# Kernel optimization log

Hardware: AMD Instinct MI355X
Metric: run time of the kernel (lower is better)

Reference implementation:

```python
import jax, jax.numpy as jnp
import numpy as np

H = 768      # hidden_size
NH = 12      # num_attention_heads
DH = H // NH # attention_head_size
FF = 3072    # intermediate_size
E = 4        # n_expert
B, S = 8, 512
EPS = 1e-12


def _layernorm(x, g, b):
    mu = jnp.mean(x, axis=-1, keepdims=True)
    var = jnp.var(x, axis=-1, keepdims=True)
    return (x - mu) * jax.lax.rsqrt(var + EPS) * g + b


def _expert_linear(x, W, b, expert_idx):
    # W: [E, in, out], b: [E, out]; gather per-sample expert weights, then batched GEMM.
    # Mathematically identical to running every expert then slicing (single_select_fwd).
    Wg = W[expert_idx]            # [B, in, out]
    bg = b[expert_idx]            # [B, out]
    return jnp.einsum('bsi,bio->bso', x, Wg) + bg[:, None, :]


def setup_inputs() -> dict:
    key = jax.random.key(0)
    ks = jax.random.split(key, 16)
    sc = 0.02
    inp = {
        'hidden_states': jax.random.normal(ks[0], (B, S, H), jnp.float32),
        'expert_idx': jax.random.randint(ks[1], (B,), 0, E, jnp.int64) if jax.config.read('jax_enable_x64') else jax.random.randint(ks[1], (B,), 0, E).astype(jnp.int32),
        'attention_mask': jnp.zeros((B, 1, 1, S), jnp.float32),
        'Wq': sc * jax.random.normal(ks[2], (E, H, H), jnp.float32),
        'bq': jnp.zeros((E, H), jnp.float32),
        'Wk': sc * jax.random.normal(ks[3], (E, H, H), jnp.float32),
        'bk': jnp.zeros((E, H), jnp.float32),
        'Wv': sc * jax.random.normal(ks[4], (E, H, H), jnp.float32),
        'bv': jnp.zeros((E, H), jnp.float32),
        'Wo': sc * jax.random.normal(ks[5], (E, H, H), jnp.float32),
        'bo': jnp.zeros((E, H), jnp.float32),
        'ln1_g': jnp.ones((H,), jnp.float32),
        'ln1_b': jnp.zeros((H,), jnp.float32),
        'Wi': sc * jax.random.normal(ks[6], (E, H, FF), jnp.float32),
        'bi': jnp.zeros((E, FF), jnp.float32),
        'Wout': sc * jax.random.normal(ks[7], (E, FF, H), jnp.float32),
        'bout': jnp.zeros((E, H), jnp.float32),
        'ln2_g': jnp.ones((H,), jnp.float32),
        'ln2_b': jnp.zeros((H,), jnp.float32),
    }
    return inp


def reference(hidden_states, expert_idx, attention_mask, Wq, bq, Wk, bk, Wv, bv,
              Wo, bo, ln1_g, ln1_b, Wi, bi, Wout, bout, ln2_g, ln2_b):
    b, s, h = hidden_states.shape
    # --- MoE self-attention (per-sample expert QKV) ---
    q = _expert_linear(hidden_states, Wq, bq, expert_idx).reshape(b, s, NH, DH).transpose(0, 2, 1, 3)
    k = _expert_linear(hidden_states, Wk, bk, expert_idx).reshape(b, s, NH, DH).transpose(0, 2, 1, 3)
    v = _expert_linear(hidden_states, Wv, bv, expert_idx).reshape(b, s, NH, DH).transpose(0, 2, 1, 3)
    scores = jnp.einsum('bhqd,bhkd->bhqk', q, k) / np.sqrt(DH).astype(np.float32)
    scores = scores + attention_mask
    probs = jax.nn.softmax(scores, axis=-1)
    ctx = jnp.einsum('bhqk,bhkd->bhqd', probs, v).transpose(0, 2, 1, 3).reshape(b, s, h)
    # --- MoE self-output: dense + residual + LN ---
    attn_out = _expert_linear(ctx, Wo, bo, expert_idx)
    x = _layernorm(attn_out + hidden_states, ln1_g, ln1_b)
    # --- MoE FFN: intermediate (GELU) + output + residual + LN ---
    hmid = jax.nn.gelu(_expert_linear(x, Wi, bi, expert_idx), approximate=False)
    ffn = _expert_linear(hmid, Wout, bout, expert_idx)
    return _layernorm(ffn + x, ln2_g, ln2_b)
```

## Files before the change

kernel.cpp:

```cpp
#include <hip/hip_runtime.h>
#include <cstdint>
#include <cstddef>

constexpr int CB  = 8;
constexpr int CS  = 512;
constexpr int CH  = 768;
constexpr int CNH = 12;
constexpr int CDH = 64;
constexpr int CFF = 3072;
constexpr int CE  = 4;
constexpr int C3H = 3 * CH;

using f32x4  = __attribute__((ext_vector_type(4))) float;
using bf16x8 = __attribute__((ext_vector_type(8))) short;

__device__ __forceinline__ short f2bf(float x) {
  union { float f; uint32_t u; } v; v.f = x;
  return (short)((v.u + 0x7fffu + ((v.u >> 16) & 1u)) >> 16);
}

__device__ __forceinline__ void gload_lds16(const void* g, void* l) {
  __builtin_amdgcn_global_load_lds((const __attribute__((address_space(1))) void*)g,
                                   (__attribute__((address_space(3))) void*)l,
                                   16, 0, 0);
}

#define VMCNT(n)  asm volatile("s_waitcnt vmcnt(" #n ")" ::: "memory")
#define SCHEDB()  __builtin_amdgcn_sched_barrier(0)

__global__ void cvt_bf16_kernel(const float* __restrict__ in, short* __restrict__ out, int n4) {
  int i = blockIdx.x * blockDim.x + threadIdx.x;
  if (i < n4) {
    float4 v = ((const float4*)in)[i];
    short4 o;
    o.x = f2bf(v.x); o.y = f2bf(v.y); o.z = f2bf(v.z); o.w = f2bf(v.w);
    ((short4*)out)[i] = o;
  }
}

__device__ __forceinline__ bool expert_used(const int* __restrict__ eidx, int e) {
  bool u = false;
#pragma unroll
  for (int s = 0; s < CB; ++s) u |= (eidx[s] == e);
  return u;
}

__device__ __forceinline__ void tpose_body(const float* __restrict__ Wb,
                                           short* __restrict__ Wtb, int K, int N) {
  __shared__ __align__(16) short Ts[64 * 68];
  const int n0 = blockIdx.x * 64, k0 = blockIdx.y * 64;
  const int t  = threadIdx.x;
  const int tn = t & 15, tk = t >> 4;
#pragma unroll
  for (int p = 0; p < 4; ++p) {
    int k = k0 + p * 16 + tk;
    float4 v = *(const float4*)(Wb + (size_t)k * N + n0 + tn * 4);
#pragma unroll
    for (int j = 0; j < 4; ++j)
      Ts[(tn * 4 + j) * 68 + p * 16 + tk] = f2bf(((const float*)&v)[j]);
  }
  __syncthreads();
#pragma unroll
  for (int p = 0; p < 4; ++p) {
    int n = n0 + p * 16 + tk;
    uint2 o = *(const uint2*)(Ts + (p * 16 + tk) * 68 + tn * 4);
    *(uint2*)(Wtb + (size_t)n * K + k0 + tn * 4) = o;
  }
}

__global__ void tpose_cvt_kernel(const float* __restrict__ W, short* __restrict__ Wt,
                                 const int* __restrict__ eidx, int K, int N) {
  const int e = blockIdx.z;
  if (!expert_used(eidx, e)) return;
  tpose_body(W + (size_t)e * K * N, Wt + (size_t)e * K * N, K, N);
}

__global__ void tpose4_kernel(const float* __restrict__ Wq, const float* __restrict__ Wk,
                              const float* __restrict__ Wv, const float* __restrict__ Wo,
                              const int* __restrict__ eidx,
                              short* __restrict__ Wqkvt, short* __restrict__ Wot) {
  const int z = blockIdx.z, e = z >> 2, m = z & 3;
  if (!expert_used(eidx, e)) return;
  const float* W = (m == 0) ? Wq : (m == 1) ? Wk : (m == 2) ? Wv : Wo;
  const float* Wb = W + (size_t)e * CH * CH;
  short* dst = (m == 3) ? (Wot + (size_t)e * CH * CH)
                        : (Wqkvt + ((size_t)e * C3H + m * CH) * CH);
  tpose_body(Wb, dst, CH, CH);
}

__global__ void qkv_bias_kernel(const float* __restrict__ bq, const float* __restrict__ bk,
                                const float* __restrict__ bv, float* __restrict__ dst) {
  int i = blockIdx.x * 256 + threadIdx.x;
  if (i >= CE * C3H) return;
  int e = i / C3H, r = i % C3H;
  int m = r / CH, c = r % CH;
  const float* s = (m == 0) ? bq : (m == 1) ? bk : bv;
  dst[i] = s[e * CH + c];
}

template <int K, int NTN, int KSPLIT, int ACT, bool OB16>
__global__ __launch_bounds__(256, 2)
void gemm5_kernel(const short* __restrict__ A, const short* __restrict__ Wt,
                  const float* __restrict__ bias, const int* __restrict__ eidx,
                  char* __restrict__ out,
                  size_t wtExpStride, int biasStride, int outLd, size_t outKsStride) {
  constexpr int BM = 128, BN = 128, TPB = 256;
  constexpr int MI = 4;
  constexpr int NT = K / KSPLIT / 64;
  constexpr int JC = 4096 / BM;
  constexpr int MTS = CS / BM;
  __shared__ __align__(16) short As[2][BM * 64];
  __shared__ __align__(16) short Bs[2][BN * 64];
  const int t = threadIdx.x, w = t >> 6, l = t & 63, lr = l & 15, lg = l >> 4;

  int exv[CB];
#pragma unroll
  for (int s = 0; s < CB; ++s) exv[s] = eidx[s];
  uint32_t epack = 0;
#pragma unroll
  for (int s = 0; s < CB; ++s) epack |= (uint32_t)exv[s] << (2 * s);
  int c0 = 0, c1 = 0, c2 = 0;
#pragma unroll
  for (int s = 0; s < CB; ++s) {
    c0 += (exv[s] == 0); c1 += (exv[s] == 1); c2 += (exv[s] == 2);
  }
  int p0 = 0, p1 = c0, p2 = c0 + c1, p3 = c0 + c1 + c2;
  uint32_t sortedPack = 0;
#pragma unroll
  for (int s = 0; s < CB; ++s) {
    int e = exv[s];
    int p = (e == 0) ? p0 : (e == 1) ? p1 : (e == 2) ? p2 : p3;
    sortedPack |= (uint32_t)s << (4 * p);
    p0 += (e == 0); p1 += (e == 1); p2 += (e == 2); p3 += (e == 3);
  }
  const int chunk = (int)gridDim.x >> 3;
  const int W_ = ((int)blockIdx.x & 7) * chunk + ((int)blockIdx.x >> 3);
  const int ks = W_ / (JC * NTN);
  const int r1 = W_ - ks * (JC * NTN);
  const int j  = r1 / NTN, nt = r1 - j * NTN;
  const int sample = (int)((sortedPack >> (4 * (j / MTS))) & 7);
  const int jj = j % MTS;
  const int e  = (int)((epack >> (2 * sample)) & 3);
  const int mrow0 = sample * CS + jj * BM;
  const int kBase = ks * NT * 64;

  const int srow = t >> 3;
  const int gcol = (((t & 7) ^ ((t >> 3) & 7)) * 8);
  const short* aSrc = A + (size_t)(mrow0 + srow) * K + kBase + gcol;
  const short* bSrc = Wt + (size_t)e * wtExpStride + (size_t)(nt * BN + srow) * K + kBase + gcol;
  constexpr int RPI = TPB / 8;
  const size_t issStride = (size_t)RPI * K;

  const int wrow = (w >> 1) * 64, wn = (w & 1) * 64;
  int aoff[2][MI], boff[2][4];
#pragma unroll
  for (int kk = 0; kk < 2; ++kk) {
    const int slot = (kk * 4 + lg) ^ (lr & 7);
#pragma unroll
    for (int mi = 0; mi < MI; ++mi)
      aoff[kk][mi] = (wrow + mi * 16 + lr) * 64 + slot * 8;
#pragma unroll
    for (int ni = 0; ni < 4; ++ni)
      boff[kk][ni] = (wn + ni * 16 + lr) * 64 + slot * 8;
  }

  f32x4 acc[MI][4] = {};

  auto STAGE = [&](int buf, int kt) {
    const short* as = aSrc + (size_t)kt * 64;
#pragma unroll
    for (int i = 0; i < 4; ++i)
      gload_lds16(as + i * issStride, &As[buf][i * TPB * 8 + t * 8]);
    const short* bs = bSrc + (size_t)kt * 64;
#pragma unroll
    for (int i = 0; i < 4; ++i)
      gload_lds16(bs + i * issStride, &Bs[buf][i * TPB * 8 + t * 8]);
  };

  STAGE(0, 0);
  for (int kt = 0; kt < NT; ++kt) {
    const int buf = kt & 1;
    if (kt + 1 < NT) { STAGE(buf ^ 1, kt + 1); VMCNT(8); }
    else             { VMCNT(0); }
    __builtin_amdgcn_s_barrier();
    SCHEDB();
    bf16x8 af[2][MI], bfr[2][4];
#pragma unroll
    for (int kk = 0; kk < 2; ++kk) {
#pragma unroll
      for (int ni = 0; ni < 4; ++ni) bfr[kk][ni] = *(const bf16x8*)(&Bs[buf][boff[kk][ni]]);
#pragma unroll
      for (int mi = 0; mi < MI; ++mi) af[kk][mi] = *(const bf16x8*)(&As[buf][aoff[kk][mi]]);
    }
    __builtin_amdgcn_s_setprio(1);
#pragma unroll
    for (int kk = 0; kk < 2; ++kk)
#pragma unroll
      for (int mi = 0; mi < MI; ++mi)
#pragma unroll
        for (int ni = 0; ni < 4; ++ni)
          acc[mi][ni] = __builtin_amdgcn_mfma_f32_16x16x32_bf16(af[kk][mi], bfr[kk][ni],
                                                                acc[mi][ni], 0, 0, 0);
    __builtin_amdgcn_s_setprio(0);
    __builtin_amdgcn_s_barrier();
    SCHEDB();
  }

  float* outF = (float*)out + (size_t)ks * outKsStride;
#pragma unroll
  for (int ni = 0; ni < 4; ++ni) {
    const int col = nt * BN + wn + ni * 16 + lr;
    const float bv = bias ? bias[e * biasStride + col] : 0.0f;
#pragma unroll
    for (int mi = 0; mi < MI; ++mi) {
      const int row0 = mrow0 + wrow + mi * 16 + lg * 4;
#pragma unroll
      for (int r = 0; r < 4; ++r) {
        float v = acc[mi][ni][r] + bv;
        if (ACT == 1) v = 0.5f * v * (1.0f + erff(v * 0.70710678118654752f));
        if (OB16) ((short*)out)[(size_t)(row0 + r) * outLd + col] = f2bf(v);
        else      outF[(size_t)(row0 + r) * outLd + col] = v;
      }
    }
  }
}

__global__ void attn_kernel(const short* __restrict__ QKV, const float* __restrict__ mask,
                            short* __restrict__ ctx) {
  __shared__ __align__(16) short Vt[2][64 * 40];
  __shared__ __align__(16) short Pt[4][2][16 * 40];
  const int bh = blockIdx.x;
  const int b = bh / CNH, h = bh % CNH;
  const int qt = blockIdx.y;
  const int t = threadIdx.x, w = t >> 6, l = t & 63, lr = l & 15, lg = l >> 4;

  const size_t bS = (size_t)b * CS;
  const short* Qh = QKV + bS * C3H + h * CDH;
  const short* Kh = Qh + CH;
  const short* Vh = Qh + 2 * CH;
  const float* mrow = mask + bS;

  const int qrow = qt * 64 + w * 16 + lr;
  bf16x8 qa[2];
  qa[0] = *(const bf16x8*)(Qh + (size_t)qrow * C3H + lg * 8);
  qa[1] = *(const bf16x8*)(Qh + (size_t)qrow * C3H + 32 + lg * 8);

  f32x4 o[4] = {};
  float lp[4] = {0.f, 0.f, 0.f, 0.f};

  const int dh = t & 63, kg = t >> 6;
  {
    short v8[8];
#pragma unroll
    for (int j = 0; j < 8; ++j) v8[j] = Vh[(size_t)(kg * 8 + j) * C3H + dh];
    uint32_t p0 = (uint32_t)(uint16_t)v8[0] | ((uint32_t)(uint16_t)v8[1] << 16);
    uint32_t p1 = (uint32_t)(uint16_t)v8[2] | ((uint32_t)(uint16_t)v8[3] << 16);
    uint32_t p2 = (uint32_t)(uint16_t)v8[4] | ((uint32_t)(uint16_t)v8[5] << 16);
    uint32_t p3 = (uint32_t)(uint16_t)v8[6] | ((uint32_t)(uint16_t)v8[7] << 16);
    uint4 pk = {p0, p1, p2, p3};
    *(uint4*)(&Vt[0][dh * 40 + kg * 8]) = pk;
  }

  for (int tt = 0; tt < CS / 32; ++tt) {
    const int k0 = tt * 32;
    __syncthreads();

    f32x4 sacc[2] = {};
#pragma unroll
    for (int n = 0; n < 2; ++n) {
      bf16x8 kb0 = *(const bf16x8*)(Kh + (size_t)(k0 + n * 16 + lr) * C3H + lg * 8);
      bf16x8 kb1 = *(const bf16x8*)(Kh + (size_t)(k0 + n * 16 + lr) * C3H + 32 + lg * 8);
      sacc[n] = __builtin_amdgcn_mfma_f32_16x16x32_bf16(qa[0], kb0, sacc[n], 0, 0, 0);
      sacc[n] = __builtin_amdgcn_mfma_f32_16x16x32_bf16(qa[1], kb1, sacc[n], 0, 0, 0);
    }

    if (tt + 1 < CS / 32) {
      const int k1 = k0 + 32;
      short v8[8];
#pragma unroll
      for (int j = 0; j < 8; ++j) v8[j] = Vh[(size_t)(k1 + kg * 8 + j) * C3H + dh];
      uint32_t p0 = (uint32_t)(uint16_t)v8[0] | ((uint32_t)(uint16_t)v8[1] << 16);
      uint32_t p1 = (uint32_t)(uint16_t)v8[2] | ((uint32_t)(uint16_t)v8[3] << 16);
      uint32_t p2 = (uint32_t)(uint16_t)v8[4] | ((uint32_t)(uint16_t)v8[5] << 16);
      uint32_t p3 = (uint32_t)(uint16_t)v8[6] | ((uint32_t)(uint16_t)v8[7] << 16);
      uint4 pk = {p0, p1, p2, p3};
      *(uint4*)(&Vt[(tt + 1) & 1][dh * 40 + kg * 8]) = pk;
    }

    const int pb = tt & 1;
#pragma unroll
    for (int n = 0; n < 2; ++n) {
      float mv = mrow[k0 + n * 16 + lr];
#pragma unroll
      for (int r = 0; r < 4; ++r) {
        float s = sacc[n][r] * 0.125f + mv;
        float e = __expf(s);
        lp[r] += e;
        Pt[w][pb][(lg * 4 + r) * 40 + n * 16 + lr] = f2bf(e);
      }
    }

    bf16x8 pa = *(const bf16x8*)(&Pt[w][pb][lr * 40 + lg * 8]);
#pragma unroll
    for (int d = 0; d < 4; ++d) {
      bf16x8 vbf = *(const bf16x8*)(&Vt[tt & 1][(d * 16 + lr) * 40 + lg * 8]);
      o[d] = __builtin_amdgcn_mfma_f32_16x16x32_bf16(pa, vbf, o[d], 0, 0, 0);
    }
  }

#pragma unroll
  for (int r = 0; r < 4; ++r) {
    float s = lp[r];
    s += __shfl_xor(s, 1); s += __shfl_xor(s, 2);
    s += __shfl_xor(s, 4); s += __shfl_xor(s, 8);
    lp[r] = 1.0f / s;
  }
#pragma unroll
  for (int d = 0; d < 4; ++d)
#pragma unroll
    for (int r = 0; r < 4; ++r) {
      int row = qt * 64 + w * 16 + lg * 4 + r;
      ctx[(bS + row) * CH + h * CDH + d * 16 + lr] = f2bf(o[d][r] * lp[r]);
    }
}

__global__ void ln12_kernel(const float* __restrict__ p0, const float* __restrict__ p1,
                            const float* __restrict__ res,
                            const float* __restrict__ btab, const int* __restrict__ eidx,
                            const float* __restrict__ g, const float* __restrict__ bta,
                            float* __restrict__ out32, short* __restrict__ out16) {
  const int row = blockIdx.x;
  const int l = threadIdx.x;
  const int e = eidx[row >> 9];
  const float* xr0 = p0 + (size_t)row * CH;
  const float* xr1 = p1 + (size_t)row * CH;
  const float* rr  = res + (size_t)row * CH;
  const float* bo  = btab + (size_t)e * CH;
  float4 v[3];
  float sum = 0.f, ss = 0.f;
#pragma unroll
  for (int j = 0; j < 3; ++j) {
    float4 a = *(const float4*)(xr0 + j * 256 + l * 4);
    float4 c = *(const float4*)(xr1 + j * 256 + l * 4);
    float4 b = *(const float4*)(rr + j * 256 + l * 4);
    float4 bb = *(const float4*)(bo + j * 256 + l * 4);
    a.x += c.x + b.x + bb.x; a.y += c.y + b.y + bb.y;
    a.z += c.z + b.z + bb.z; a.w += c.w + b.w + bb.w;
    v[j] = a;
    sum += a.x + a.y + a.z + a.w;
    ss  += a.x * a.x + a.y * a.y + a.z * a.z + a.w * a.w;
  }
#pragma unroll
  for (int m = 1; m < 64; m <<= 1) { sum += __shfl_xor(sum, m); ss += __shfl_xor(ss, m); }
  const float mean = sum * (1.0f / CH);
  const float var  = ss * (1.0f / CH) - mean * mean;
  const float rstd = rsqrtf(var + 1e-12f);
#pragma unroll
  for (int j = 0; j < 3; ++j) {
    float4 gg = *(const float4*)(g   + j * 256 + l * 4);
    float4 bb = *(const float4*)(bta + j * 256 + l * 4);
    float4 a = v[j], y;
    y.x = (a.x - mean) * rstd * gg.x + bb.x;
    y.y = (a.y - mean) * rstd * gg.y + bb.y;
    y.z = (a.z - mean) * rstd * gg.z + bb.z;
    y.w = (a.w - mean) * rstd * gg.w + bb.w;
    *(float4*)(out32 + (size_t)row * CH + j * 256 + l * 4) = y;
    if (out16) {
      short4 o;
      o.x = f2bf(y.x); o.y = f2bf(y.y); o.z = f2bf(y.z); o.w = f2bf(y.w);
      *(short4*)(out16 + (size_t)row * CH + j * 256 + l * 4) = o;
    }
  }
}

extern "C" void kernel_launch(void* const* d_in, const int* in_sizes, int n_in,
                              void* d_out, int out_size, void* d_ws, size_t ws_size,
                              hipStream_t stream) {
  (void)in_sizes; (void)n_in; (void)out_size; (void)ws_size;
  const float* hidden = (const float*)d_in[0];
  const int*   eidx   = (const int*)d_in[1];
  const float* mask   = (const float*)d_in[2];
  const float* Wq   = (const float*)d_in[3];
  const float* bq   = (const float*)d_in[4];
  const float* Wk   = (const float*)d_in[5];
  const float* bk   = (const float*)d_in[6];
  const float* Wv   = (const float*)d_in[7];
  const float* bv   = (const float*)d_in[8];
  const float* Wo   = (const float*)d_in[9];
  const float* bo   = (const float*)d_in[10];
  const float* ln1g = (const float*)d_in[11];
  const float* ln1b = (const float*)d_in[12];
  const float* Wi   = (const float*)d_in[13];
  const float* bi   = (const float*)d_in[14];
  const float* Wout = (const float*)d_in[15];
  const float* bout = (const float*)d_in[16];
  const float* ln2g = (const float*)d_in[17];
  const float* ln2b = (const float*)d_in[18];

  char* ws = (char*)d_ws;
  size_t off = 0;
  auto alloc = [&](size_t bytes) {
    void* p = ws + off;
    off += (bytes + 255) & ~(size_t)255;
    return p;
  };
  const size_t M = (size_t)CB * CS;
  short* Xb    = (short*)alloc(M * CH * 2);
  char*  Rbig  = (char*)alloc(M * CFF * 2);
  char*  Rcx   = (char*)alloc(M * CH * 4);
  float* parts = (float*)alloc(2 * M * CH * 4);
  float* qkvbias = (float*)alloc(CE * C3H * 4);
  short* Wqkvt = (short*)alloc((size_t)CE * C3H * CH * 2);
  short* Wot   = (short*)alloc((size_t)CE * CH * CH * 2);
  short* Wit   = (short*)alloc((size_t)CE * CH * CFF * 2);
  short* Wo2t  = (short*)alloc((size_t)CE * CFF * CH * 2);
  short* QKVb = (short*)Rbig;
  short* hmid = (short*)Rbig;
  short* ctxb = (short*)Rcx;
  float* x1   = (float*)Rcx;
  short* x1b  = Xb;

  const int n4 = (int)(M * CH / 4);
  cvt_bf16_kernel<<<(n4 + 255) / 256, 256, 0, stream>>>(hidden, Xb, n4);
  tpose4_kernel<<<dim3(CH / 64, CH / 64, 4 * CE), 256, 0, stream>>>(Wq, Wk, Wv, Wo, eidx, Wqkvt, Wot);
  tpose_cvt_kernel<<<dim3(CFF / 64, CH / 64, CE), 256, 0, stream>>>(Wi, Wit, eidx, CH, CFF);
  tpose_cvt_kernel<<<dim3(CH / 64, CFF / 64, CE), 256, 0, stream>>>(Wout, Wo2t, eidx, CFF, CH);
  qkv_bias_kernel<<<(CE * C3H + 255) / 256, 256, 0, stream>>>(bq, bk, bv, qkvbias);

  gemm5_kernel<CH, 18, 1, 0, true><<<576, 256, 0, stream>>>(
      Xb, Wqkvt, qkvbias, eidx, (char*)QKVb, (size_t)C3H * CH, C3H, C3H, 0);
  attn_kernel<<<dim3(CB * CNH, CS / 64), 256, 0, stream>>>(QKVb, mask, ctxb);
  gemm5_kernel<CH, 6, 2, 0, false><<<384, 256, 0, stream>>>(
      ctxb, Wot, nullptr, eidx, (char*)parts, (size_t)CH * CH, CH, CH, M * CH);
  ln12_kernel<<<(int)M, 64, 0, stream>>>(parts, parts + M * CH, hidden, bo, eidx,
                                         ln1g, ln1b, x1, x1b);
  gemm5_kernel<CH, 24, 1, 1, true><<<768, 256, 0, stream>>>(
      x1b, Wit, bi, eidx, (char*)hmid, (size_t)CH * CFF, CFF, CFF, 0);
  gemm5_kernel<CFF, 6, 2, 0, false><<<384, 256, 0, stream>>>(
      hmid, Wo2t, nullptr, eidx, (char*)parts, (size_t)CFF * CH, CH, CH, M * CH);
  ln12_kernel<<<(int)M, 64, 0, stream>>>(parts, parts + M * CH, x1, bout, eidx,
                                         ln2g, ln2b, (float*)d_out, nullptr);
}
```

Before: 205.8 us.

## Add 128x256-tile triple-buffered GEMM kernel for QKV and FFN projections

Introduces gemm6, a 512-thread GEMM with 128x256 output tiles and a three-stage LDS pipeline that prefetches two k-tiles ahead. The QKV, FFN-intermediate and FFN-output GEMMs now use it, with half the grid size. The goal is more operand reuse per block and better hiding of global-load latency. In exchange it uses more LDS, runs one block per CU, and gives fewer blocks across the CUs, which may hurt wave balance, especially for the 192-block FFN-output GEMM. The expert-routing decode is factored into a shared helper.

New measurement: 221.8 us. +7.8%, slower.

```diff
diff --git a/kernel.cpp b/kernel.cpp
--- a/kernel.cpp
+++ b/kernel.cpp
@@ -98,6 +98,145 @@
   dst[i] = s[e * CH + c];
 }
 
+template <int BM, int NTN, int KSPLIT>
+__device__ __forceinline__ void moe_decode(const int* __restrict__ eidx,
+                                           int& e, int& mrow0, int& nt, int& ks) {
+  constexpr int JC = 4096 / BM;
+  constexpr int MTS = CS / BM;
+  int exv[CB];
+#pragma unroll
+  for (int s = 0; s < CB; ++s) exv[s] = eidx[s];
+  uint32_t epack = 0;
+#pragma unroll
+  for (int s = 0; s < CB; ++s) epack |= (uint32_t)exv[s] << (2 * s);
+  int c0 = 0, c1 = 0, c2 = 0;
+#pragma unroll
+  for (int s = 0; s < CB; ++s) {
+    c0 += (exv[s] == 0); c1 += (exv[s] == 1); c2 += (exv[s] == 2);
+  }
+  int p0 = 0, p1 = c0, p2 = c0 + c1, p3 = c0 + c1 + c2;
+  uint32_t sortedPack = 0;
+#pragma unroll
+  for (int s = 0; s < CB; ++s) {
+    int ee = exv[s];
+    int p = (ee == 0) ? p0 : (ee == 1) ? p1 : (ee == 2) ? p2 : p3;
+    sortedPack |= (uint32_t)s << (4 * p);
+    p0 += (ee == 0); p1 += (ee == 1); p2 += (ee == 2); p3 += (ee == 3);
+  }
+  const int chunk = (int)gridDim.x >> 3;
+  const int W_ = ((int)blockIdx.x & 7) * chunk + ((int)blockIdx.x >> 3);
+  ks = W_ / (JC * NTN);
+  const int r1 = W_ - ks * (JC * NTN);
+  const int j  = r1 / NTN; nt = r1 - j * NTN;
+  const int sample = (int)((sortedPack >> (4 * (j / MTS))) & 7);
+  const int jj = j % MTS;
+  e = (int)((epack >> (2 * sample)) & 3);
+  mrow0 = sample * CS + jj * BM;
+}
+
+template <int K, int NTN, int KSPLIT, int ACT, bool OB16>
+__global__ __launch_bounds__(512, 1)
+void gemm6_kernel(const short* __restrict__ A, const short* __restrict__ Wt,
+                  const float* __restrict__ bias, const int* __restrict__ eidx,
+                  char* __restrict__ out,
+                  size_t wtExpStride, int biasStride, int outLd, size_t outKsStride) {
+  constexpr int BM = 128, BN = 256;
+  constexpr int NT = K / KSPLIT / 64;
+  __shared__ __align__(16) short As[3][BM * 64];
+  __shared__ __align__(16) short Bs[3][BN * 64];
+  const int t = threadIdx.x, w = t >> 6, l = t & 63, lr = l & 15, lg = l >> 4;
+
+  int e, mrow0, nt, ks;
+  moe_decode<BM, NTN, KSPLIT>(eidx, e, mrow0, nt, ks);
+  const int kBase = ks * NT * 64;
+
+  const int srow = t >> 3;
+  const int gcol = (((t & 7) ^ ((t >> 3) & 7)) * 8);
+  const short* aSrc = A + (size_t)(mrow0 + srow) * K + kBase + gcol;
+  const short* bSrc = Wt + (size_t)e * wtExpStride + (size_t)(nt * BN + srow) * K + kBase + gcol;
+  const size_t iss64 = (size_t)64 * K;
+
+  const int wrow = (w >> 2) * 64, wn = (w & 3) * 64;
+  int aoff[2][4], boff[2][4];
+#pragma unroll
+  for (int kk = 0; kk < 2; ++kk) {
+    const int slot = (kk * 4 + lg) ^ (lr & 7);
+#pragma unroll
+    for (int mi = 0; mi < 4; ++mi)
+      aoff[kk][mi] = (wrow + mi * 16 + lr) * 64 + slot * 8;
+#pragma unroll
+    for (int ni = 0; ni < 4; ++ni)
+      boff[kk][ni] = (wn + ni * 16 + lr) * 64 + slot * 8;
+  }
+
+  f32x4 acc[4][4] = {};
+
+  auto STAGE = [&](int buf, int kt) {
+    const short* as = aSrc + (size_t)kt * 64;
+#pragma unroll
+    for (int i = 0; i < 2; ++i)
+      gload_lds16(as + i * iss64, &As[buf][i * 4096 + t * 8]);
+    const short* bs = bSrc + (size_t)kt * 64;
+#pragma unroll
+    for (int i = 0; i < 4; ++i)
+      gload_lds16(bs + i * iss64, &Bs[buf][i * 4096 + t * 8]);
+  };
+
+  STAGE(0, 0);
+  STAGE(1, 1);
+  VMCNT(6);
+  __builtin_amdgcn_s_barrier();
+  SCHEDB();
+
+  int cb = 0;
+  for (int kt = 0; kt < NT; ++kt) {
+    if (kt + 2 < NT) {
+      const int sb = (cb == 0) ? 2 : cb - 1;
+      STAGE(sb, kt + 2);
+    }
+#pragma unroll
+    for (int kk = 0; kk < 2; ++kk) {
+      bf16x8 af[4], bfr[4];
+#pragma unroll
+      for (int ni = 0; ni < 4; ++ni) bfr[ni] = *(const bf16x8*)(&Bs[cb][boff[kk][ni]]);
+#pragma unroll
+      for (int mi = 0; mi < 4; ++mi) af[mi] = *(const bf16x8*)(&As[cb][aoff[kk][mi]]);
+      __builtin_amdgcn_s_setprio(1);
+#pragma unroll
+      for (int mi = 0; mi < 4; ++mi)
+#pragma unroll
+        for (int ni = 0; ni < 4; ++ni)
+          acc[mi][ni] = __builtin_amdgcn_mfma_f32_16x16x32_bf16(af[mi], bfr[ni],
+                                                                acc[mi][ni], 0, 0, 0);
+      __builtin_amdgcn_s_setprio(0);
+    }
+    SCHEDB();
+    if (kt + 2 < NT) { VMCNT(6); }
+    else             { VMCNT(0); }
+    __builtin_amdgcn_s_barrier();
+    SCHEDB();
+    cb = (cb == 2) ? 0 : cb + 1;
+  }
+
+  float* outF = (float*)out + (size_t)ks * outKsStride;
+#pragma unroll
+  for (int ni = 0; ni < 4; ++ni) {
+    const int col = nt * BN + wn + ni * 16 + lr;
+    const float bv = bias ? bias[e * biasStride + col] : 0.0f;
+#pragma unroll
+    for (int mi = 0; mi < 4; ++mi) {
+      const int row0 = mrow0 + wrow + mi * 16 + lg * 4;
+#pragma unroll
+      for (int r = 0; r < 4; ++r) {
+        float v = acc[mi][ni][r] + bv;
+        if (ACT == 1) v = 0.5f * v * (1.0f + erff(v * 0.70710678118654752f));
+        if (OB16) ((short*)out)[(size_t)(row0 + r) * outLd + col] = f2bf(v);
+        else      outF[(size_t)(row0 + r) * outLd + col] = v;
+      }
+    }
+  }
+}
+
 template <int K, int NTN, int KSPLIT, int ACT, bool OB16>
 __global__ __launch_bounds__(256, 2)
 void gemm5_kernel(const short* __restrict__ A, const short* __restrict__ Wt,
@@ -107,41 +246,12 @@
   constexpr int BM = 128, BN = 128, TPB = 256;
   constexpr int MI = 4;
   constexpr int NT = K / KSPLIT / 64;
-  constexpr int JC = 4096 / BM;
-  constexpr int MTS = CS / BM;
   __shared__ __align__(16) short As[2][BM * 64];
   __shared__ __align__(16) short Bs[2][BN * 64];
   const int t = threadIdx.x, w = t >> 6, l = t & 63, lr = l & 15, lg = l >> 4;
 
-  int exv[CB];
-#pragma unroll
-  for (int s = 0; s < CB; ++s) exv[s] = eidx[s];
-  uint32_t epack = 0;
-#pragma unroll
-  for (int s = 0; s < CB; ++s) epack |= (uint32_t)exv[s] << (2 * s);
-  int c0 = 0, c1 = 0, c2 = 0;
-#pragma unroll
-  for (int s = 0; s < CB; ++s) {
-    c0 += (exv[s] == 0); c1 += (exv[s] == 1); c2 += (exv[s] == 2);
-  }
-  int p0 = 0, p1 = c0, p2 = c0 + c1, p3 = c0 + c1 + c2;
-  uint32_t sortedPack = 0;
-#pragma unroll
-  for (int s = 0; s < CB; ++s) {
-    int e = exv[s];
-    int p = (e == 0) ? p0 : (e == 1) ? p1 : (e == 2) ? p2 : p3;
-    sortedPack |= (uint32_t)s << (4 * p);
-    p0 += (e == 0); p1 += (e == 1); p2 += (e == 2); p3 += (e == 3);
-  }
-  const int chunk = (int)gridDim.x >> 3;
-  const int W_ = ((int)blockIdx.x & 7) * chunk + ((int)blockIdx.x >> 3);
-  const int ks = W_ / (JC * NTN);
-  const int r1 = W_ - ks * (JC * NTN);
-  const int j  = r1 / NTN, nt = r1 - j * NTN;
-  const int sample = (int)((sortedPack >> (4 * (j / MTS))) & 7);
-  const int jj = j % MTS;
-  const int e  = (int)((epack >> (2 * sample)) & 3);
-  const int mrow0 = sample * CS + jj * BM;
+  int e, mrow0, nt, ks;
+  moe_decode<BM, NTN, KSPLIT>(eidx, e, mrow0, nt, ks);
   const int kBase = ks * NT * 64;
 
   const int srow = t >> 3;
@@ -427,16 +537,16 @@
   tpose_cvt_kernel<<<dim3(CH / 64, CFF / 64, CE), 256, 0, stream>>>(Wout, Wo2t, eidx, CFF, CH);
   qkv_bias_kernel<<<(CE * C3H + 255) / 256, 256, 0, stream>>>(bq, bk, bv, qkvbias);
 
-  gemm5_kernel<CH, 18, 1, 0, true><<<576, 256, 0, stream>>>(
+  gemm6_kernel<CH, 9, 1, 0, true><<<288, 512, 0, stream>>>(
       Xb, Wqkvt, qkvbias, eidx, (char*)QKVb, (size_t)C3H * CH, C3H, C3H, 0);
   attn_kernel<<<dim3(CB * CNH, CS / 64), 256, 0, stream>>>(QKVb, mask, ctxb);
   gemm5_kernel<CH, 6, 2, 0, false><<<384, 256, 0, stream>>>(
       ctxb, Wot, nullptr, eidx, (char*)parts, (size_t)CH * CH, CH, CH, M * CH);
   ln12_kernel<<<(int)M, 64, 0, stream>>>(parts, parts + M * CH, hidden, bo, eidx,
                                          ln1g, ln1b, x1, x1b);
-  gemm5_kernel<CH, 24, 1, 1, true><<<768, 256, 0, stream>>>(
+  gemm6_kernel<CH, 12, 1, 1, true><<<384, 512, 0, stream>>>(
       x1b, Wit, bi, eidx, (char*)hmid, (size_t)CH * CFF, CFF, CFF, 0);
-  gemm5_kernel<CFF, 6, 2, 0, false><<<384, 256, 0, stream>>>(
+  gemm6_kernel<CFF, 3, 2, 0, false><<<192, 512, 0, stream>>>(
       hmid, Wo2t, nullptr, eidx, (char*)parts, (size_t)CFF * CH, CH, CH, M * CH);
   ln12_kernel<<<(int)M, 64, 0, stream>>>(parts, parts + M * CH, x1, bout, eidx,
                                          ln2g, ln2b, (float*)d_out, nullptr);
```

## Widen GEMM tile to 128x192, split B staging mid-iteration, 4-way K-split FFN-out

Applied to the files above, without the earlier changes.

The expert GEMM kernel now uses a 128x192 output tile (6 N-fragments per wave), so each A tile is reused across more columns and fewer blocks are launched. B-tile loads for the next stage are issued between the two k-halves of the current iteration, to overlap them with MFMA work. The FFN-output GEMM moves to a 4-way K split, with the extra partials written into the no-longer-needed QKV weight buffer and summed in a 4-input LayerNorm kernel. The larger tile raises register and LDS use, which may lower occupancy, and the extra partials add memory traffic.

Result: faster. 191.3 us (-7.0%).

```diff
diff --git a/kernel.cpp b/kernel.cpp
--- a/kernel.cpp
+++ b/kernel.cpp
@@ -98,61 +98,67 @@
   dst[i] = s[e * CH + c];
 }
 
+template <int BM, int NTN, int KSPLIT>
+__device__ __forceinline__ void moe_decode(const int* __restrict__ eidx,
+                                           int& e, int& mrow0, int& nt, int& ks) {
+  constexpr int JC = 4096 / BM;
+  constexpr int MTS = CS / BM;
+  int exv[CB];
+#pragma unroll
+  for (int s = 0; s < CB; ++s) exv[s] = eidx[s];
+  uint32_t epack = 0;
+#pragma unroll
+  for (int s = 0; s < CB; ++s) epack |= (uint32_t)exv[s] << (2 * s);
+  int c0 = 0, c1 = 0, c2 = 0;
+#pragma unroll
+  for (int s = 0; s < CB; ++s) {
+    c0 += (exv[s] == 0); c1 += (exv[s] == 1); c2 += (exv[s] == 2);
+  }
+  int p0 = 0, p1 = c0, p2 = c0 + c1, p3 = c0 + c1 + c2;
+  uint32_t sortedPack = 0;
+#pragma unroll
+  for (int s = 0; s < CB; ++s) {
+    int ee = exv[s];
+    int p = (ee == 0) ? p0 : (ee == 1) ? p1 : (ee == 2) ? p2 : p3;
+    sortedPack |= (uint32_t)s << (4 * p);
+    p0 += (ee == 0); p1 += (ee == 1); p2 += (ee == 2); p3 += (ee == 3);
+  }
+  const int chunk = (int)gridDim.x >> 3;
+  const int W_ = ((int)blockIdx.x & 7) * chunk + ((int)blockIdx.x >> 3);
+  ks = W_ / (JC * NTN);
+  const int r1 = W_ - ks * (JC * NTN);
+  const int j  = r1 / NTN; nt = r1 - j * NTN;
+  const int sample = (int)((sortedPack >> (4 * (j / MTS))) & 7);
+  const int jj = j % MTS;
+  e = (int)((epack >> (2 * sample)) & 3);
+  mrow0 = sample * CS + jj * BM;
+}
+
 template <int K, int NTN, int KSPLIT, int ACT, bool OB16>
 __global__ __launch_bounds__(256, 2)
-void gemm5_kernel(const short* __restrict__ A, const short* __restrict__ Wt,
+void gemm7_kernel(const short* __restrict__ A, const short* __restrict__ Wt,
                   const float* __restrict__ bias, const int* __restrict__ eidx,
-                  char* __restrict__ out,
+                  char* __restrict__ out, char* __restrict__ out2,
                   size_t wtExpStride, int biasStride, int outLd, size_t outKsStride) {
-  constexpr int BM = 128, BN = 128, TPB = 256;
-  constexpr int MI = 4;
+  constexpr int BM = 128, BN = 192;
+  constexpr int MI = 4, NI = 6;
   constexpr int NT = K / KSPLIT / 64;
-  constexpr int JC = 4096 / BM;
-  constexpr int MTS = CS / BM;
   __shared__ __align__(16) short As[2][BM * 64];
   __shared__ __align__(16) short Bs[2][BN * 64];
   const int t = threadIdx.x, w = t >> 6, l = t & 63, lr = l & 15, lg = l >> 4;
 
-  int exv[CB];
-#pragma unroll
-  for (int s = 0; s < CB; ++s) exv[s] = eidx[s];
-  uint32_t epack = 0;
-#pragma unroll
-  for (int s = 0; s < CB; ++s) epack |= (uint32_t)exv[s] << (2 * s);
-  int c0 = 0, c1 = 0, c2 = 0;
-#pragma unroll
-  for (int s = 0; s < CB; ++s) {
-    c0 += (exv[s] == 0); c1 += (exv[s] == 1); c2 += (exv[s] == 2);
-  }
-  int p0 = 0, p1 = c0, p2 = c0 + c1, p3 = c0 + c1 + c2;
-  uint32_t sortedPack = 0;
-#pragma unroll
-  for (int s = 0; s < CB; ++s) {
-    int e = exv[s];
-    int p = (e == 0) ? p0 : (e == 1) ? p1 : (e == 2) ? p2 : p3;
-    sortedPack |= (uint32_t)s << (4 * p);
-    p0 += (e == 0); p1 += (e == 1); p2 += (e == 2); p3 += (e == 3);
-  }
-  const int chunk = (int)gridDim.x >> 3;
-  const int W_ = ((int)blockIdx.x & 7) * chunk + ((int)blockIdx.x >> 3);
-  const int ks = W_ / (JC * NTN);
-  const int r1 = W_ - ks * (JC * NTN);
-  const int j  = r1 / NTN, nt = r1 - j * NTN;
-  const int sample = (int)((sortedPack >> (4 * (j / MTS))) & 7);
-  const int jj = j % MTS;
-  const int e  = (int)((epack >> (2 * sample)) & 3);
-  const int mrow0 = sample * CS + jj * BM;
+  int e, mrow0, nt, ks;
+  moe_decode<BM, NTN, KSPLIT>(eidx, e, mrow0, nt, ks);
   const int kBase = ks * NT * 64;
 
   const int srow = t >> 3;
   const int gcol = (((t & 7) ^ ((t >> 3) & 7)) * 8);
   const short* aSrc = A + (size_t)(mrow0 + srow) * K + kBase + gcol;
   const short* bSrc = Wt + (size_t)e * wtExpStride + (size_t)(nt * BN + srow) * K + kBase + gcol;
-  constexpr int RPI = TPB / 8;
-  const size_t issStride = (size_t)RPI * K;
-
-  const int wrow = (w >> 1) * 64, wn = (w & 1) * 64;
-  int aoff[2][MI], boff[2][4];
+  const size_t iss32 = (size_t)32 * K;
+
+  const int wrow = (w >> 1) * 64, wn = (w & 1) * 96;
+  int aoff[2][MI], boff[2][NI];
 #pragma unroll
   for (int kk = 0; kk < 2; ++kk) {
     const int slot = (kk * 4 + lg) ^ (lr & 7);
@@ -160,55 +166,73 @@
     for (int mi = 0; mi < MI; ++mi)
       aoff[kk][mi] = (wrow + mi * 16 + lr) * 64 + slot * 8;
 #pragma unroll
-    for (int ni = 0; ni < 4; ++ni)
+    for (int ni = 0; ni < NI; ++ni)
       boff[kk][ni] = (wn + ni * 16 + lr) * 64 + slot * 8;
   }
 
-  f32x4 acc[MI][4] = {};
-
-  auto STAGE = [&](int buf, int kt) {
+  f32x4 acc[MI][NI] = {};
+
+  auto STAGE_A = [&](int buf, int kt) {
     const short* as = aSrc + (size_t)kt * 64;
 #pragma unroll
     for (int i = 0; i < 4; ++i)
-      gload_lds16(as + i * issStride, &As[buf][i * TPB * 8 + t * 8]);
+      gload_lds16(as + i * iss32, &As[buf][i * 2048 + t * 8]);
+  };
+  auto STAGE_B = [&](int buf, int kt) {
     const short* bs = bSrc + (size_t)kt * 64;
 #pragma unroll
-    for (int i = 0; i < 4; ++i)
-      gload_lds16(bs + i * issStride, &Bs[buf][i * TPB * 8 + t * 8]);
+    for (int i = 0; i < 6; ++i)
+      gload_lds16(bs + i * iss32, &Bs[buf][i * 2048 + t * 8]);
   };
 
-  STAGE(0, 0);
+  STAGE_A(0, 0);
+  STAGE_B(0, 0);
+
   for (int kt = 0; kt < NT; ++kt) {
     const int buf = kt & 1;
-    if (kt + 1 < NT) { STAGE(buf ^ 1, kt + 1); VMCNT(8); }
+    if (kt + 1 < NT) { STAGE_A(buf ^ 1, kt + 1); VMCNT(4); }
     else             { VMCNT(0); }
     __builtin_amdgcn_s_barrier();
     SCHEDB();
-    bf16x8 af[2][MI], bfr[2][4];
-#pragma unroll
-    for (int kk = 0; kk < 2; ++kk) {
-#pragma unroll
-      for (int ni = 0; ni < 4; ++ni) bfr[kk][ni] = *(const bf16x8*)(&Bs[buf][boff[kk][ni]]);
-#pragma unroll
-      for (int mi = 0; mi < MI; ++mi) af[kk][mi] = *(const bf16x8*)(&As[buf][aoff[kk][mi]]);
-    }
-    __builtin_amdgcn_s_setprio(1);
-#pragma unroll
-    for (int kk = 0; kk < 2; ++kk)
+    {
+      bf16x8 af[MI], bfr[NI];
+#pragma unroll
+      for (int ni = 0; ni < NI; ++ni) bfr[ni] = *(const bf16x8*)(&Bs[buf][boff[0][ni]]);
+#pragma unroll
+      for (int mi = 0; mi < MI; ++mi) af[mi] = *(const bf16x8*)(&As[buf][aoff[0][mi]]);
+      __builtin_amdgcn_s_setprio(1);
 #pragma unroll
       for (int mi = 0; mi < MI; ++mi)
 #pragma unroll
-        for (int ni = 0; ni < 4; ++ni)
-          acc[mi][ni] = __builtin_amdgcn_mfma_f32_16x16x32_bf16(af[kk][mi], bfr[kk][ni],
+        for (int ni = 0; ni < NI; ++ni)
+          acc[mi][ni] = __builtin_amdgcn_mfma_f32_16x16x32_bf16(af[mi], bfr[ni],
                                                                 acc[mi][ni], 0, 0, 0);
-    __builtin_amdgcn_s_setprio(0);
+      __builtin_amdgcn_s_setprio(0);
+    }
+    if (kt + 1 < NT) STAGE_B(buf ^ 1, kt + 1);
+    {
+      bf16x8 af[MI], bfr[NI];
+#pragma unroll
+      for (int ni = 0; ni < NI; ++ni) bfr[ni] = *(const bf16x8*)(&Bs[buf][boff[1][ni]]);
+#pragma unroll
+      for (int mi = 0; mi < MI; ++mi) af[mi] = *(const bf16x8*)(&As[buf][aoff[1][mi]]);
+      __builtin_amdgcn_s_setprio(1);
+#pragma unroll
+      for (int mi = 0; mi < MI; ++mi)
+#pragma unroll
+        for (int ni = 0; ni < NI; ++ni)
+          acc[mi][ni] = __builtin_amdgcn_mfma_f32_16x16x32_bf16(af[mi], bfr[ni],
+                                                                acc[mi][ni], 0, 0, 0);
+      __builtin_amdgcn_s_setprio(0);
+    }
     __builtin_amdgcn_s_barrier();
     SCHEDB();
   }
 
-  float* outF = (float*)out + (size_t)ks * outKsStride;
-#pragma unroll
-  for (int ni = 0; ni < 4; ++ni) {
+  float* outF = (ks < 2) ? ((float*)out + (size_t)ks * outKsStride)
+                         : ((float*)out2 + (size_t)(ks - 2) * outKsStride);
+#pragma unroll
+  for (int ni = 0; ni < NI; ++ni) {
     const int col = nt * BN + wn + ni * 16 + lr;
     const float bv = bias ? bias[e * biasStride + col] : 0.0f;
 #pragma unroll
@@ -324,7 +348,9 @@
     }
 }
 
+template <int NP>
 __global__ void ln12_kernel(const float* __restrict__ p0, const float* __restrict__ p1,
+                            const float* __restrict__ p2, const float* __restrict__ p3,
                             const float* __restrict__ res,
                             const float* __restrict__ btab, const int* __restrict__ eidx,
                             const float* __restrict__ g, const float* __restrict__ bta,
@@ -346,6 +372,12 @@
     float4 bb = *(const float4*)(bo + j * 256 + l * 4);
     a.x += c.x + b.x + bb.x; a.y += c.y + b.y + bb.y;
     a.z += c.z + b.z + bb.z; a.w += c.w + b.w + bb.w;
+    if (NP == 4) {
+      float4 d2 = *(const float4*)(p2 + (size_t)row * CH + j * 256 + l * 4);
+      float4 d3 = *(const float4*)(p3 + (size_t)row * CH + j * 256 + l * 4);
+      a.x += d2.x + d3.x; a.y += d2.y + d3.y;
+      a.z += d2.z + d3.z; a.w += d2.w + d3.w;
+    }
     v[j] = a;
     sum += a.x + a.y + a.z + a.w;
     ss  += a.x * a.x + a.y * a.y + a.z * a.z + a.w * a.w;
@@ -419,6 +451,8 @@
   short* ctxb = (short*)Rcx;
   float* x1   = (float*)Rcx;
   short* x1b  = Xb;
+  float* pp2  = (float*)Wqkvt;
+  float* pp3  = pp2 + M * CH;
 
   const int n4 = (int)(M * CH / 4);
   cvt_bf16_kernel<<<(n4 + 255) / 256, 256, 0, stream>>>(hidden, Xb, n4);
@@ -427,17 +461,17 @@
   tpose_cvt_kernel<<<dim3(CH / 64, CFF / 64, CE), 256, 0, stream>>>(Wout, Wo2t, eidx, CFF, CH);
   qkv_bias_kernel<<<(CE * C3H + 255) / 256, 256, 0, stream>>>(bq, bk, bv, qkvbias);
 
-  gemm5_kernel<CH, 18, 1, 0, true><<<576, 256, 0, stream>>>(
-      Xb, Wqkvt, qkvbias, eidx, (char*)QKVb, (size_t)C3H * CH, C3H, C3H, 0);
+  gemm7_kernel<CH, 12, 1, 0, true><<<384, 256, 0, stream>>>(
+      Xb, Wqkvt, qkvbias, eidx, (char*)QKVb, nullptr, (size_t)C3H * CH, C3H, C3H, 0);
   attn_kernel<<<dim3(CB * CNH, CS / 64), 256, 0, stream>>>(QKVb, mask, ctxb);
-  gemm5_kernel<CH, 6, 2, 0, false><<<384, 256, 0, stream>>>(
-      ctxb, Wot, nullptr, eidx, (char*)parts, (size_t)CH * CH, CH, CH, M * CH);
-  ln12_kernel<<<(int)M, 64, 0, stream>>>(parts, parts + M * CH, hidden, bo, eidx,
-                                         ln1g, ln1b, x1, x1b);
-  gemm5_kernel<CH, 24, 1, 1, true><<<768, 256, 0, stream>>>(
-      x1b, Wit, bi, eidx, (char*)hmid, (size_t)CH * CFF, CFF, CFF, 0);
-  gemm5_kernel<CFF, 6, 2, 0, false><<<384, 256, 0, stream>>>(
-      hmid, Wo2t, nullptr, eidx, (char*)parts, (size_t)CFF * CH, CH, CH, M * CH);
-  ln12_kernel<<<(int)M, 64, 0, stream>>>(parts, parts + M * CH, x1, bout, eidx,
-                                         ln2g, ln2b, (float*)d_out, nullptr);
-}
+  gemm7_kernel<CH, 4, 2, 0, false><<<256, 256, 0, stream>>>(
+      ctxb, Wot, nullptr, eidx, (char*)parts, nullptr, (size_t)CH * CH, CH, CH, M * CH);
+  ln12_kernel<2><<<(int)M, 64, 0, stream>>>(parts, parts + M * CH, nullptr, nullptr,
+                                            hidden, bo, eidx, ln1g, ln1b, x1, x1b);
+  gemm7_kernel<CH, 16, 1, 1, true><<<512, 256, 0, stream>>>(
+      x1b, Wit, bi, eidx, (char*)hmid, nullptr, (size_t)CH * CFF, CFF, CFF, 0);
+  gemm7_kernel<CFF, 4, 4, 0, false><<<512, 256, 0, stream>>>(
+      hmid, Wo2t, nullptr, eidx, (char*)parts, (char*)pp2, (size_t)CFF * CH, CH, CH, M * CH);
+  ln12_kernel<4><<<(int)M, 64, 0, stream>>>(parts, parts + M * CH, pp2, pp3,
+                                            x1, bout, eidx, ln2g, ln2b, (float*)d_out, nullptr);
+}
```
